# Performance work log

Hardware: AMD Instinct MI355X
Metric: run time of the kernel (lower is better)

Reference implementation:

```python
import jax, jax.numpy as jnp
import numpy as np

COST_CLASS = 1.0
COST_BBOX = 5.0
COST_GIOU = 2.0
BS, NQ, NC, M = 16, 1000, 92, 1024


def box_cxcywh_to_xyxy(x):
    xc, yc, w, h = jnp.split(x, 4, axis=-1)
    return jnp.concatenate([xc - 0.5 * w, yc - 0.5 * h, xc + 0.5 * w, yc + 0.5 * h], axis=-1)


def generalized_box_iou(a, b):
    # a: [N,4] xyxy, b: [M,4] xyxy -> [N,M]
    area_a = (a[:, 2] - a[:, 0]) * (a[:, 3] - a[:, 1])
    area_b = (b[:, 2] - b[:, 0]) * (b[:, 3] - b[:, 1])
    lt = jnp.maximum(a[:, None, :2], b[None, :, :2])  # [N,M,2]
    rb = jnp.minimum(a[:, None, 2:], b[None, :, 2:])
    wh = jnp.clip(rb - lt, 0.0)
    inter = wh[..., 0] * wh[..., 1]
    union = area_a[:, None] + area_b[None, :] - inter
    iou = inter / union
    lt_e = jnp.minimum(a[:, None, :2], b[None, :, :2])
    rb_e = jnp.maximum(a[:, None, 2:], b[None, :, 2:])
    wh_e = jnp.clip(rb_e - lt_e, 0.0)
    area_e = wh_e[..., 0] * wh_e[..., 1]
    return iou - (area_e - union) / area_e


def setup_inputs() -> dict:
    key = jax.random.key(0)
    k1, k2, k3, k4 = jax.random.split(key, 4)
    return {
        'pred_logits': jax.random.normal(k1, (BS, NQ, NC), dtype=jnp.float32),
        'pred_boxes': jax.random.uniform(k2, (BS, NQ, 4), dtype=jnp.float32),
        'tgt_boxes': jax.random.uniform(k3, (M, 4), dtype=jnp.float32),
        'tgt_labels': jax.random.randint(k4, (M,), 0, NC),
    }


def reference(pred_logits, pred_boxes, tgt_boxes, tgt_labels):
    bs, nq, nc = pred_logits.shape
    out_prob = jax.nn.softmax(pred_logits.reshape(bs * nq, nc), axis=-1)
    out_bbox = pred_boxes.reshape(bs * nq, 4)
    tgt_ids = jnp.clip(tgt_labels, 0, nc - 1)
    # classification cost: -prob of target class, gathered per target -> [N, M]
    cost_class = -out_prob[:, tgt_ids]
    # L1 cdist on cxcywh boxes -> [N, M]
    cost_bbox = jnp.abs(out_bbox[:, None, :] - tgt_bbox_b(tgt_boxes)[None, :, :]).sum(-1)
    cost_giou = -generalized_box_iou(box_cxcywh_to_xyxy(out_bbox), box_cxcywh_to_xyxy(tgt_boxes))
    C = COST_BBOX * cost_bbox + COST_CLASS * cost_class + COST_GIOU * cost_giou
    return C.reshape(bs, nq, -1)


def tgt_bbox_b(tgt_boxes):
    return tgt_boxes
```

## Files before the change

### kernel.cpp

```cpp
#include <hip/hip_runtime.h>
#include <math.h>


#define NROWS 16000
#define NC 92
#define M_TGT 1024
#define TPB 256
#define ROWS 8
#define KPT 4

__global__ __launch_bounds__(TPB) void hungarian_cost_kernel(
    const float* __restrict__ logits,
    const float* __restrict__ pboxes,
    const float* __restrict__ tboxes,
    const int*   __restrict__ tlabels,
    float* __restrict__ out)
{
    const int n0 = blockIdx.x * ROWS;
    const int t = threadIdx.x;
    const int lane = t & 63;
    const int wid  = t >> 6;

    __shared__ float prob[ROWS][NC];
    __shared__ float rowv[ROWS][12];

    float tcx[KPT], tcy[KPT], twd[KPT], tht[KPT];
    float bx0[KPT], by0[KPT], bx1[KPT], by1[KPT], areab[KPT];
    int   lbl[KPT];
    #pragma unroll
    for (int k = 0; k < KPT; ++k) {
        const float4 tb = reinterpret_cast<const float4*>(tboxes)[t + k * TPB];
        tcx[k] = tb.x; tcy[k] = tb.y; twd[k] = tb.z; tht[k] = tb.w;
        bx0[k] = tb.x - 0.5f * tb.z;  by0[k] = tb.y - 0.5f * tb.w;
        bx1[k] = tb.x + 0.5f * tb.z;  by1[k] = tb.y + 0.5f * tb.w;
        areab[k] = (bx1[k] - bx0[k]) * (by1[k] - by0[k]);
        int L = tlabels[t + k * TPB];
        lbl[k] = (L < 0) ? 0 : (L > NC - 1 ? NC - 1 : L);
    }

    #pragma unroll
    for (int rr = 0; rr < 2; ++rr) {
        const int r = wid * 2 + rr;
        const float* lg = logits + (size_t)(n0 + r) * NC;
        const float x0 = lg[lane];
        const bool  hi = (lane < NC - 64);
        const float x1 = hi ? lg[64 + lane] : -INFINITY;
        float mx = fmaxf(x0, x1);
        #pragma unroll
        for (int off = 32; off >= 1; off >>= 1)
            mx = fmaxf(mx, __shfl_xor(mx, off));
        const float e0 = __expf(x0 - mx);
        const float e1 = hi ? __expf(x1 - mx) : 0.0f;
        float s = e0 + e1;
        #pragma unroll
        for (int off = 32; off >= 1; off >>= 1)
            s += __shfl_xor(s, off);
        const float rs = __builtin_amdgcn_rcpf(s);
        prob[r][lane] = e0 * rs;
        if (hi) prob[r][64 + lane] = e1 * rs;
    }

    if (t < ROWS) {
        const float4 pb = reinterpret_cast<const float4*>(pboxes)[n0 + t];
        const float ax0 = pb.x - 0.5f * pb.z, ay0 = pb.y - 0.5f * pb.w;
        const float ax1 = pb.x + 0.5f * pb.z, ay1 = pb.y + 0.5f * pb.w;
        rowv[t][0] = ax0; rowv[t][1] = ay0; rowv[t][2] = ax1; rowv[t][3] = ay1;
        rowv[t][4] = (ax1 - ax0) * (ay1 - ay0);
        rowv[t][5] = pb.x; rowv[t][6] = pb.y; rowv[t][7] = pb.z; rowv[t][8] = pb.w;
    }
    __syncthreads();

    #pragma unroll 2
    for (int r = 0; r < ROWS; ++r) {
        const float ax0 = rowv[r][0], ay0 = rowv[r][1];
        const float ax1 = rowv[r][2], ay1 = rowv[r][3];
        const float area_a = rowv[r][4];
        const float pcx = rowv[r][5], pcy = rowv[r][6];
        const float pw  = rowv[r][7], ph  = rowv[r][8];
        float* __restrict__ orow = out + (size_t)(n0 + r) * M_TGT + t;
        #pragma unroll
        for (int k = 0; k < KPT; ++k) {
            const float cls = prob[r][lbl[k]];
            const float cb = fabsf(pcx - tcx[k]) + fabsf(pcy - tcy[k])
                           + fabsf(pw - twd[k]) + fabsf(ph - tht[k]);
            const float iwu = fminf(ax1, bx1[k]) - fmaxf(ax0, bx0[k]);
            const float ihu = fminf(ay1, by1[k]) - fmaxf(ay0, by0[k]);
            const float inter = fmaxf(iwu, 0.0f) * fmaxf(ihu, 0.0f);
            const float uni = area_a + areab[k] - inter;
            const float ew = pw + twd[k] - iwu;
            const float eh = ph + tht[k] - ihu;
            const float ae = ew * eh;
            const float iou  = inter * __builtin_amdgcn_rcpf(uni);
            const float covg = uni   * __builtin_amdgcn_rcpf(ae);
            orow[k * TPB] = 5.0f * cb - cls - 2.0f * iou - 2.0f * covg + 2.0f;
        }
    }
}

extern "C" void kernel_launch(void* const* d_in, const int* in_sizes, int n_in,
                              void* d_out, int out_size, void* d_ws, size_t ws_size,
                              hipStream_t stream) {
    const float* logits  = (const float*)d_in[0];
    const float* pboxes  = (const float*)d_in[1];
    const float* tboxes  = (const float*)d_in[2];
    const int*   tlabels = (const int*)d_in[3];
    float* out = (float*)d_out;

    hungarian_cost_kernel<<<NROWS / ROWS, TPB, 0, stream>>>(
        logits, pboxes, tboxes, tlabels, out);
}
```

Baseline: 25.30 us.

## Vectorize output stores as float4 and double rows per block

Each thread now owns four contiguous targets, so its four outputs go out as one float4 store per row instead of four strided scalar stores. Labels are loaded as one int4. Rows per block go from 8 to 16, which halves the grid and amortizes the per-thread target setup over more rows. The constant +2 is folded into the shared softmax table as 2 - p, and box areas use w*h directly, which trims a few ALU ops at some small risk of floating-point differences.

```diff
diff --git a/kernel.cpp b/kernel.cpp
--- a/kernel.cpp
+++ b/kernel.cpp
@@ -6,7 +6,7 @@
 #define NC 92
 #define M_TGT 1024
 #define TPB 256
-#define ROWS 8
+#define ROWS 16
 #define KPT 4
 
 __global__ __launch_bounds__(TPB) void hungarian_cost_kernel(
@@ -21,26 +21,26 @@
     const int lane = t & 63;
     const int wid  = t >> 6;
 
-    __shared__ float prob[ROWS][NC];
+    __shared__ float negp[ROWS][NC];
     __shared__ float rowv[ROWS][12];
 
     float tcx[KPT], tcy[KPT], twd[KPT], tht[KPT];
     float bx0[KPT], by0[KPT], bx1[KPT], by1[KPT], areab[KPT];
-    int   lbl[KPT];
+    const int4 lb4 = reinterpret_cast<const int4*>(tlabels)[t];
+    int lbl[KPT] = {lb4.x, lb4.y, lb4.z, lb4.w};
     #pragma unroll
     for (int k = 0; k < KPT; ++k) {
-        const float4 tb = reinterpret_cast<const float4*>(tboxes)[t + k * TPB];
+        const float4 tb = reinterpret_cast<const float4*>(tboxes)[4 * t + k];
         tcx[k] = tb.x; tcy[k] = tb.y; twd[k] = tb.z; tht[k] = tb.w;
         bx0[k] = tb.x - 0.5f * tb.z;  by0[k] = tb.y - 0.5f * tb.w;
         bx1[k] = tb.x + 0.5f * tb.z;  by1[k] = tb.y + 0.5f * tb.w;
-        areab[k] = (bx1[k] - bx0[k]) * (by1[k] - by0[k]);
-        int L = tlabels[t + k * TPB];
-        lbl[k] = (L < 0) ? 0 : (L > NC - 1 ? NC - 1 : L);
+        areab[k] = tb.z * tb.w;
+        lbl[k] = (lbl[k] < 0) ? 0 : (lbl[k] > NC - 1 ? NC - 1 : lbl[k]);
     }
 
     #pragma unroll
-    for (int rr = 0; rr < 2; ++rr) {
-        const int r = wid * 2 + rr;
+    for (int j = 0; j < 4; ++j) {
+        const int r = wid * 4 + j;
         const float* lg = logits + (size_t)(n0 + r) * NC;
         const float x0 = lg[lane];
         const bool  hi = (lane < NC - 64);
@@ -56,44 +56,44 @@
         for (int off = 32; off >= 1; off >>= 1)
             s += __shfl_xor(s, off);
         const float rs = __builtin_amdgcn_rcpf(s);
-        prob[r][lane] = e0 * rs;
-        if (hi) prob[r][64 + lane] = e1 * rs;
+        negp[r][lane] = fmaf(-e0, rs, 2.0f);
+        if (hi) negp[r][64 + lane] = fmaf(-e1, rs, 2.0f);
     }
 
     if (t < ROWS) {
         const float4 pb = reinterpret_cast<const float4*>(pboxes)[n0 + t];
-        const float ax0 = pb.x - 0.5f * pb.z, ay0 = pb.y - 0.5f * pb.w;
-        const float ax1 = pb.x + 0.5f * pb.z, ay1 = pb.y + 0.5f * pb.w;
-        rowv[t][0] = ax0; rowv[t][1] = ay0; rowv[t][2] = ax1; rowv[t][3] = ay1;
-        rowv[t][4] = (ax1 - ax0) * (ay1 - ay0);
-        rowv[t][5] = pb.x; rowv[t][6] = pb.y; rowv[t][7] = pb.z; rowv[t][8] = pb.w;
+        rowv[t][0] = pb.x; rowv[t][1] = pb.y; rowv[t][2] = pb.z; rowv[t][3] = pb.w;
+        rowv[t][4] = pb.x - 0.5f * pb.z;  rowv[t][5] = pb.y - 0.5f * pb.w;
+        rowv[t][6] = pb.x + 0.5f * pb.z;  rowv[t][7] = pb.y + 0.5f * pb.w;
+        rowv[t][8] = pb.z * pb.w;
     }
     __syncthreads();
 
-    #pragma unroll 2
+    float* obase = out + (size_t)n0 * M_TGT + 4 * t;
+    #pragma unroll
     for (int r = 0; r < ROWS; ++r) {
-        const float ax0 = rowv[r][0], ay0 = rowv[r][1];
-        const float ax1 = rowv[r][2], ay1 = rowv[r][3];
-        const float area_a = rowv[r][4];
-        const float pcx = rowv[r][5], pcy = rowv[r][6];
-        const float pw  = rowv[r][7], ph  = rowv[r][8];
-        float* __restrict__ orow = out + (size_t)(n0 + r) * M_TGT + t;
+        const float4 pc = *reinterpret_cast<const float4*>(&rowv[r][0]);
+        const float4 pe = *reinterpret_cast<const float4*>(&rowv[r][4]);
+        const float area_a = rowv[r][8];
+        float tmp[KPT];
         #pragma unroll
         for (int k = 0; k < KPT; ++k) {
-            const float cls = prob[r][lbl[k]];
-            const float cb = fabsf(pcx - tcx[k]) + fabsf(pcy - tcy[k])
-                           + fabsf(pw - twd[k]) + fabsf(ph - tht[k]);
-            const float iwu = fminf(ax1, bx1[k]) - fmaxf(ax0, bx0[k]);
-            const float ihu = fminf(ay1, by1[k]) - fmaxf(ay0, by0[k]);
+            const float cls2 = negp[r][lbl[k]];
+            const float cb = fabsf(pc.x - tcx[k]) + fabsf(pc.y - tcy[k])
+                           + fabsf(pc.z - twd[k]) + fabsf(pc.w - tht[k]);
+            const float iwu = fminf(pe.z, bx1[k]) - fmaxf(pe.x, bx0[k]);
+            const float ihu = fminf(pe.w, by1[k]) - fmaxf(pe.y, by0[k]);
             const float inter = fmaxf(iwu, 0.0f) * fmaxf(ihu, 0.0f);
             const float uni = area_a + areab[k] - inter;
-            const float ew = pw + twd[k] - iwu;
-            const float eh = ph + tht[k] - ihu;
+            const float ew = pc.z + twd[k] - iwu;
+            const float eh = pc.w + tht[k] - ihu;
             const float ae = ew * eh;
-            const float iou  = inter * __builtin_amdgcn_rcpf(uni);
-            const float covg = uni   * __builtin_amdgcn_rcpf(ae);
-            orow[k * TPB] = 5.0f * cb - cls - 2.0f * iou - 2.0f * covg + 2.0f;
+            tmp[k] = fmaf(5.0f, cb, cls2)
+                   - 2.0f * inter * __builtin_amdgcn_rcpf(uni)
+                   - 2.0f * uni   * __builtin_amdgcn_rcpf(ae);
         }
+        float4 res = {tmp[0], tmp[1], tmp[2], tmp[3]};
+        *reinterpret_cast<float4*>(obase + (size_t)r * M_TGT) = res;
     }
 }
 
```

Measured after the change: 25.76 us. Within noise of the previous version (+1.8%).
